# Kernel optimization log

Measured on AMD Instinct MI355X. Metric: run time of the kernel, lower is better.

## Reference

```python
import jax, jax.numpy as jnp
import numpy as np
import math


def _dct2_mat(N):
    # DCT-II matrix, norm=None convention of torch_dct: X[k] = 2*sum_n x[n]*cos(pi*(2n+1)*k/(2N))
    n = np.arange(N)
    k = n[:, None]
    C = 2.0 * np.cos(np.pi * (2 * n[None, :] + 1) * k / (2 * N))
    return jnp.asarray(C, dtype=jnp.float32)


def setup_inputs() -> dict:
    key = jax.random.key(0)
    k1, k2, k3 = jax.random.split(key, 3)
    B, H, W = 128, 256, 256
    thresh = int(H / (2 * math.sqrt(2)))  # 90
    x = jax.random.normal(k1, (B, 3, H, W), dtype=jnp.float32)
    w = jax.random.normal(k2, (1, thresh), dtype=jnp.float32) * 0.05
    b = jax.random.normal(k3, (1,), dtype=jnp.float32) * 0.05
    return {"x": x, "w": w, "b": b}


def reference(x, w, b):
    B, C, H, W = x.shape
    Ch = _dct2_mat(H)
    Cw = _dct2_mat(W)
    # dct_2d: DCT-II along last two dims
    xd = jnp.einsum('bchw,kw->bchk', x, Cw)
    xd = jnp.einsum('bchk,jh->bcjk', xd, Ch)
    xd = jax.lax.stop_gradient(xd)  # original does x.detach() inside get_fft_feature
    gray = 0.2989 * xd[:, 0] + 0.587 * xd[:, 1] + 0.114 * xd[:, 2]  # [B,H,W]
    F = jnp.fft.fft2(gray, axes=(-2, -1))
    re = F.real + 1e-8  # original adds epsilon to both real and imag parts
    im = F.imag + 1e-8
    mag = jnp.log(jnp.sqrt(re * re + im * im + 1e-10) + 1e-10)
    mag = jnp.fft.fftshift(mag, axes=(-2, -1))  # quadrant-swap `shift` == fftshift for even dims
    # radial binning (static integer radii, as in azimuthalAverage)
    yy, xx = np.indices([H, W])
    r = np.sqrt((xx - H / 2) ** 2 + (yy - W / 2) ** 2).astype(np.int32).ravel()
    nbins = int(r.max()) + 1
    nr = jnp.asarray(np.bincount(r, minlength=nbins).astype(np.float32))
    rj = jnp.asarray(r)
    tbin = jax.vmap(lambda m: jax.ops.segment_sum(m, rj, num_segments=nbins))(mag.reshape(B, -1))
    prof = tbin / (nr + 1e-10)  # [B, nbins]
    prof = prof[:, 1:-2]  # azimuthalAverage returns radial_prof[1:-2]
    mn = jnp.min(prof, axis=1, keepdims=True)
    mx = jnp.max(prof, axis=1, keepdims=True)
    out = (prof - mn) / (mx - mn)
    out = jnp.where(jnp.isnan(out), 0.0, out)
    thresh = w.shape[1]
    feat = out[:, -thresh:]  # [B, thresh]
    return feat @ w.T + b  # [B, 1]
```

## Files before the change

### kernel.cpp

```cpp
#include <hip/hip_runtime.h>
#include <math.h>

#define NBINS 182
#define NB 128

typedef unsigned short u16;
typedef __attribute__((ext_vector_type(8))) short short8;
typedef __attribute__((ext_vector_type(4))) float f32x4;

__device__ __forceinline__ u16 f2bf(float f) {
    union { float f; unsigned u; } v; v.f = f;
    unsigned r = v.u + 0x7FFF + ((v.u >> 16) & 1);
    return (u16)(r >> 16);
}
__device__ __forceinline__ float bf2f(u16 u) {
    union { unsigned u; float f; } v; v.u = ((unsigned)u) << 16;
    return v.f;
}
__device__ __forceinline__ short8 negbf(short8 v) {
    short8 r;
#pragma unroll
    for (int i = 0; i < 8; ++i) r[i] = v[i] ^ (short)0x8000;
    return r;
}

__device__ __forceinline__ int radial_bin(int dx, int dy) {
    return (int)sqrtf((float)(dx * dx + dy * dy));
}

__global__ __launch_bounds__(256) void prep(const float* __restrict__ x,
                                            u16* __restrict__ G,
                                            float* __restrict__ M_re,
                                            float* __restrict__ M_im,
                                            u16* __restrict__ A1,
                                            float* __restrict__ nrpart,
                                            float* __restrict__ tbin) {
    __shared__ double ctab[1024];
    __shared__ double stab[1024];
    __shared__ float s[NBINS];
    int blk = blockIdx.x;
    int t = threadIdx.x;

    if (blk < 256) {
        for (int i = t; i < 1024; i += 256) {
            double a = 3.14159265358979323846 * (double)i / 512.0;
            ctab[i] = cos(a);
            stab[i] = sin(a);
        }
        __syncthreads();
        int j = blk;
        int w = t;
        double re = 0.0, im = 0.0;
        int tw = 2 * w + 1;
        for (int k = 0; k < 256; ++k) {
            int e = (4 * j * k) & 1023;
            int m = (tw * k) & 1023;
            double cw = 2.0 * ctab[m];
            re += ctab[e] * cw;
            im -= stab[e] * cw;
        }
        M_re[j * 256 + w] = (float)re;
        M_im[j * 256 + w] = (float)im;
        A1[j * 256 + w] = f2bf((float)re);
        A1[(j + 256) * 256 + w] = f2bf((float)im);
    } else if (blk < 512) {
        int i = blk - 256;
        if (t < NBINS) s[t] = 0.0f;
        __syncthreads();
        int bin = radial_bin(t - 128, i - 128);
        atomicAdd(&s[bin], 1.0f);
        __syncthreads();
        if (t < NBINS) nrpart[t * 256 + i] = s[t];
    } else if (blk < 544) {
        int idx = (blk - 512) * 256 + t;
        for (int i = idx; i < NB * NBINS; i += 32 * 256) tbin[i] = 0.0f;
    } else {
        int tid = (blk - 544) * 256 + t;
        for (int i = tid; i < 2097152; i += 262144) {
            int idx = i * 4;
            int b = idx >> 16;
            int rem = idx & 65535;
            const float* p = x + (size_t)b * 196608 + rem;
            float4 r = *(const float4*)p;
            float4 g = *(const float4*)(p + 65536);
            float4 bl = *(const float4*)(p + 131072);
            float g0 = 0.2989f * r.x + 0.587f * g.x + 0.114f * bl.x;
            float g1 = 0.2989f * r.y + 0.587f * g.y + 0.114f * bl.y;
            float g2 = 0.2989f * r.z + 0.587f * g.z + 0.114f * bl.z;
            float g3 = 0.2989f * r.w + 0.587f * g.w + 0.114f * bl.w;
            uint2 o;
            o.x = (unsigned)f2bf(g0) | ((unsigned)f2bf(g1) << 16);
            o.y = (unsigned)f2bf(g2) | ((unsigned)f2bf(g3) << 16);
            *(uint2*)(G + idx) = o;
        }
    }
}

__global__ __launch_bounds__(256) void s1(const u16* __restrict__ A1,
                                          const u16* __restrict__ G,
                                          u16* __restrict__ Tt_re,
                                          u16* __restrict__ Tt_im) {
    __shared__ u16 As[128 * 40];
    __shared__ u16 Bs[128 * 40];
    __shared__ u16 Cs[64 * 136];
    int b = blockIdx.z;
    int r0 = blockIdx.y * 128;
    int h0 = blockIdx.x * 128;
    int t = threadIdx.x;
    int lane = t & 63, wv = t >> 6;
    int wr = (wv >> 1) * 64;
    int wc = (wv & 1) * 64;
    int fr = lane & 15;
    int fk = (lane >> 4) << 3;

    f32x4 acc[4][4];
#pragma unroll
    for (int i = 0; i < 4; ++i)
#pragma unroll
        for (int j = 0; j < 4; ++j) acc[i][j] = (f32x4){0.f, 0.f, 0.f, 0.f};

    const u16* Ap = A1 + (size_t)r0 * 256;
    const u16* Gp = G + (size_t)b * 65536 + (size_t)h0 * 256;

    for (int kk = 0; kk < 256; kk += 32) {
#pragma unroll
        for (int c = t; c < 512; c += 256) {
            int row = c >> 2, off = (c & 3) << 3;
            *(uint4*)&As[row * 40 + off] =
                *(const uint4*)(Ap + (size_t)row * 256 + kk + off);
            *(uint4*)&Bs[row * 40 + off] =
                *(const uint4*)(Gp + (size_t)row * 256 + kk + off);
        }
        __syncthreads();
        short8 af[4], bfr[4];
#pragma unroll
        for (int i = 0; i < 4; ++i)
            af[i] = *(const short8*)&As[(wr + i * 16 + fr) * 40 + fk];
#pragma unroll
        for (int j = 0; j < 4; ++j)
            bfr[j] = *(const short8*)&Bs[(wc + j * 16 + fr) * 40 + fk];
#pragma unroll
        for (int i = 0; i < 4; ++i)
#pragma unroll
            for (int j = 0; j < 4; ++j)
                acc[i][j] = __builtin_amdgcn_mfma_f32_16x16x32_bf16(
                    af[i], bfr[j], acc[i][j], 0, 0, 0);
        __syncthreads();
    }

    u16* dstp = ((r0 < 256) ? Tt_re : Tt_im) + (size_t)b * 65536
              + (size_t)(r0 & 255) * 256 + h0;
    int rq = (lane >> 4) << 2;
#pragma unroll
    for (int pass = 0; pass < 2; ++pass) {
        if ((wr >> 6) == pass) {
#pragma unroll
            for (int i = 0; i < 4; ++i)
#pragma unroll
                for (int j = 0; j < 4; ++j) {
                    int col = wc + j * 16 + fr;
#pragma unroll
                    for (int reg = 0; reg < 4; ++reg) {
                        int lrow = i * 16 + rq + reg;
                        Cs[lrow * 136 + col] = f2bf(acc[i][j][reg]);
                    }
                }
        }
        __syncthreads();
        for (int idx = t; idx < 1024; idx += 256) {
            int row = idx >> 4, k = idx & 15;
            *(uint4*)(dstp + (size_t)(pass * 64 + row) * 256 + k * 8) =
                *(const uint4*)&Cs[row * 136 + k * 8];
        }
        __syncthreads();
    }
}

__global__ __launch_bounds__(256) void s2f(const u16* __restrict__ A1,
                                           const float* __restrict__ M_re,
                                           const u16* __restrict__ Tt_re,
                                           const u16* __restrict__ Tt_im,
                                           float* __restrict__ tbin) {
    __shared__ u16 Ar[64 * 40], Ai[64 * 40], Br[64 * 40], Bi[64 * 40];
    __shared__ float sbins[NBINS];
    __shared__ float sM[256];
    int blk = blockIdx.x;
    int t = threadIdx.x;

    if (blk >= 1024) {
        int b = blk - 1024;
        sM[t] = M_re[128 * 256 + t];
        __syncthreads();
        if (t > 128) return;
        const u16* pr = Tt_re + (size_t)b * 65536 + (size_t)t * 256;
        const u16* pi = Tt_im + (size_t)b * 65536 + (size_t)t * 256;
        float re = 0.0f, im = 0.0f;
        for (int h = 0; h < 256; h += 8) {
            uint4 vr = *(const uint4*)(pr + h);
            uint4 vi = *(const uint4*)(pi + h);
            unsigned wr[4] = {vr.x, vr.y, vr.z, vr.w};
            unsigned wi[4] = {vi.x, vi.y, vi.z, vi.w};
#pragma unroll
            for (int q = 0; q < 4; ++q) {
                re = fmaf(sM[h + 2 * q], bf2f((u16)(wr[q] & 0xffff)), re);
                re = fmaf(sM[h + 2 * q + 1], bf2f((u16)(wr[q] >> 16)), re);
                im = fmaf(sM[h + 2 * q], bf2f((u16)(wi[q] & 0xffff)), im);
                im = fmaf(sM[h + 2 * q + 1], bf2f((u16)(wi[q] >> 16)), im);
            }
        }
        re += 1e-8f; im += 1e-8f;
        float mag = __logf(sqrtf(re * re + im * im + 1e-10f) + 1e-10f);
        float wj = (t == 0 || t == 128) ? 1.0f : 2.0f;
        int dx = (t < 128) ? t : t - 256;
        int bin = radial_bin(dx, -128);
        atomicAdd(&tbin[b * NBINS + bin], wj * mag);
        return;
    }

    int b = blk >> 3;
    int u0 = ((blk >> 2) & 1) * 64;
    int j0 = (blk & 3) * 64;
    int lane = t & 63, wv = t >> 6;
    int wu = (wv >> 1) * 32;
    int wj = (wv & 1) * 32;
    int fr = lane & 15;
    int fk = (lane >> 4) << 3;

    for (int i = t; i < NBINS; i += 256) sbins[i] = 0.0f;

    f32x4 accr[2][2], acci[2][2];
#pragma unroll
    for (int i = 0; i < 2; ++i)
#pragma unroll
        for (int j = 0; j < 2; ++j) {
            accr[i][j] = (f32x4){0.f, 0.f, 0.f, 0.f};
            acci[i][j] = (f32x4){0.f, 0.f, 0.f, 0.f};
        }

    const u16* Apr = A1 + (size_t)u0 * 256;
    const u16* Api = A1 + (size_t)(256 + u0) * 256;
    const u16* Tr = Tt_re + (size_t)b * 65536 + (size_t)j0 * 256;
    const u16* Ti = Tt_im + (size_t)b * 65536 + (size_t)j0 * 256;

    int lrow = t >> 2, loff = (t & 3) << 3;

    for (int kk = 0; kk < 256; kk += 32) {
        *(uint4*)&Ar[lrow * 40 + loff] =
            *(const uint4*)(Apr + (size_t)lrow * 256 + kk + loff);
        *(uint4*)&Ai[lrow * 40 + loff] =
            *(const uint4*)(Api + (size_t)lrow * 256 + kk + loff);
        *(uint4*)&Br[lrow * 40 + loff] =
            *(const uint4*)(Tr + (size_t)lrow * 256 + kk + loff);
        *(uint4*)&Bi[lrow * 40 + loff] =
            *(const uint4*)(Ti + (size_t)lrow * 256 + kk + loff);
        __syncthreads();
        short8 arf[2], aif[2], naif[2], brf[2], bif[2];
#pragma unroll
        for (int i = 0; i < 2; ++i) {
            arf[i] = *(const short8*)&Ar[(wu + i * 16 + fr) * 40 + fk];
            aif[i] = *(const short8*)&Ai[(wu + i * 16 + fr) * 40 + fk];
            naif[i] = negbf(aif[i]);
        }
#pragma unroll
        for (int j = 0; j < 2; ++j) {
            brf[j] = *(const short8*)&Br[(wj + j * 16 + fr) * 40 + fk];
            bif[j] = *(const short8*)&Bi[(wj + j * 16 + fr) * 40 + fk];
        }
#pragma unroll
        for (int i = 0; i < 2; ++i)
#pragma unroll
            for (int j = 0; j < 2; ++j) {
                accr[i][j] = __builtin_amdgcn_mfma_f32_16x16x32_bf16(
                    arf[i], brf[j], accr[i][j], 0, 0, 0);
                accr[i][j] = __builtin_amdgcn_mfma_f32_16x16x32_bf16(
                    naif[i], bif[j], accr[i][j], 0, 0, 0);
                acci[i][j] = __builtin_amdgcn_mfma_f32_16x16x32_bf16(
                    arf[i], bif[j], acci[i][j], 0, 0, 0);
                acci[i][j] = __builtin_amdgcn_mfma_f32_16x16x32_bf16(
                    aif[i], brf[j], acci[i][j], 0, 0, 0);
            }
        __syncthreads();
    }

    int rq = (lane >> 4) << 2;
#pragma unroll
    for (int i = 0; i < 2; ++i)
#pragma unroll
        for (int j = 0; j < 2; ++j) {
            int v = j0 + wj + j * 16 + fr;
            int dx = (v < 128) ? v : v - 256;
            int dx2 = dx * dx;
#pragma unroll
            for (int reg = 0; reg < 4; ++reg) {
                int u = u0 + wu + i * 16 + rq + reg;
                float wrow = (u == 0) ? 1.0f : 2.0f;
                int bin = (int)sqrtf((float)(dx2 + u * u));
                float re = accr[i][j][reg] + 1e-8f;
                float im = acci[i][j][reg] + 1e-8f;
                float mag = __logf(sqrtf(re * re + im * im + 1e-10f) + 1e-10f);
                atomicAdd(&sbins[bin], wrow * mag);
            }
        }
    __syncthreads();
    for (int i = t; i < NBINS; i += 256)
        atomicAdd(&tbin[b * NBINS + i], sbins[i]);
}

__global__ __launch_bounds__(192) void finalize(const float* __restrict__ tbin,
                                                const float* __restrict__ nrpart,
                                                const float* __restrict__ w,
                                                const float* __restrict__ bias,
                                                float* __restrict__ out) {
    __shared__ float prof[NBINS];
    __shared__ float smn, smx, ssum;
    int b = blockIdx.x;
    int t = threadIdx.x;
    if (t < NBINS) {
        const float4* p = (const float4*)(nrpart + t * 256);
        float4 a = {0.f, 0.f, 0.f, 0.f};
        for (int i = 0; i < 64; ++i) {
            float4 v = p[i];
            a.x += v.x; a.y += v.y; a.z += v.z; a.w += v.w;
        }
        float nr = (a.x + a.y) + (a.z + a.w);
        prof[t] = tbin[b * NBINS + t] / (nr + 1e-10f);
    }
    __syncthreads();
    if (t == 0) {
        float mn = prof[1], mx = prof[1];
        for (int i = 2; i <= 179; ++i) {
            float p = prof[i];
            mn = fminf(mn, p);
            mx = fmaxf(mx, p);
        }
        smn = mn; smx = mx; ssum = 0.0f;
    }
    __syncthreads();
    if (t < 90) {
        float denom = smx - smn;
        float v = (prof[90 + t] - smn) / denom;
        if (v != v) v = 0.0f;
        atomicAdd(&ssum, v * w[t]);
    }
    __syncthreads();
    if (t == 0) out[b] = ssum + bias[0];
}

extern "C" void kernel_launch(void* const* d_in, const int* in_sizes, int n_in,
                              void* d_out, int out_size, void* d_ws, size_t ws_size,
                              hipStream_t stream) {
    const float* x = (const float*)d_in[0];
    const float* w = (const float*)d_in[1];
    const float* bias = (const float*)d_in[2];
    float* out = (float*)d_out;

    float* M_re = (float*)d_ws;
    float* M_im = M_re + 65536;
    u16* A1 = (u16*)(M_im + 65536);
    u16* G = A1 + 131072;
    u16* Tt_re = G + (size_t)NB * 65536;
    u16* Tt_im = Tt_re + (size_t)NB * 65536;
    float* tbin = (float*)(Tt_im + (size_t)NB * 65536);
    float* nrpart = tbin + NB * NBINS;

    prep<<<1568, 256, 0, stream>>>(x, G, M_re, M_im, A1, nrpart, tbin);
    s1<<<dim3(2, 4, NB), 256, 0, stream>>>(A1, G, Tt_re, Tt_im);
    s2f<<<1152, 256, 0, stream>>>(A1, M_re, Tt_re, Tt_im, tbin);
    finalize<<<NB, 192, 0, stream>>>(tbin, nrpart, w, bias, out);
}
```

Baseline: 233.4 us.

## Fuse grayscale into first DCT GEMM and finalize into second stage

The grayscale bf16 conversion moves out of the prep kernel and into the s1 GEMM's B-tile load, so the intermediate G buffer is no longer written and re-read. s1 now stores its results straight from the accumulators to global memory instead of staging them through LDS. The finalize kernel is merged into s2f: each block bumps a per-batch counter and the last one computes the profile and output. The trade-offs are that x is re-read by each row-tile block, the stores become narrow and scattered, and the completion counter adds atomics and fences.

Measured after the change: 317.9 us. 36.2% more time.

```diff
diff --git a/kernel.cpp b/kernel.cpp
--- a/kernel.cpp
+++ b/kernel.cpp
@@ -28,13 +28,12 @@
     return (int)sqrtf((float)(dx * dx + dy * dy));
 }
 
-__global__ __launch_bounds__(256) void prep(const float* __restrict__ x,
-                                            u16* __restrict__ G,
-                                            float* __restrict__ M_re,
+__global__ __launch_bounds__(256) void prep(float* __restrict__ M_re,
                                             float* __restrict__ M_im,
                                             u16* __restrict__ A1,
                                             float* __restrict__ nrpart,
-                                            float* __restrict__ tbin) {
+                                            float* __restrict__ tbin,
+                                            int* __restrict__ cnt) {
     __shared__ double ctab[1024];
     __shared__ double stab[1024];
     __shared__ float s[NBINS];
@@ -71,16 +70,51 @@
         atomicAdd(&s[bin], 1.0f);
         __syncthreads();
         if (t < NBINS) nrpart[t * 256 + i] = s[t];
-    } else if (blk < 544) {
+    } else {
         int idx = (blk - 512) * 256 + t;
         for (int i = idx; i < NB * NBINS; i += 32 * 256) tbin[i] = 0.0f;
-    } else {
-        int tid = (blk - 544) * 256 + t;
-        for (int i = tid; i < 2097152; i += 262144) {
-            int idx = i * 4;
-            int b = idx >> 16;
-            int rem = idx & 65535;
-            const float* p = x + (size_t)b * 196608 + rem;
+        if (blk == 512 && t < NB) cnt[t] = 0;
+    }
+}
+
+__global__ __launch_bounds__(256) void s1(const float* __restrict__ x,
+                                          const u16* __restrict__ A1,
+                                          u16* __restrict__ Tt_re,
+                                          u16* __restrict__ Tt_im) {
+    __shared__ u16 As[128 * 40];
+    __shared__ u16 Bs[128 * 40];
+    int b = blockIdx.z;
+    int r0 = blockIdx.y * 128;
+    int h0 = blockIdx.x * 128;
+    int t = threadIdx.x;
+    int lane = t & 63, wv = t >> 6;
+    int wr = (wv >> 1) * 64;
+    int wc = (wv & 1) * 64;
+    int fr = lane & 15;
+    int fk = (lane >> 4) << 3;
+
+    f32x4 acc[4][4];
+#pragma unroll
+    for (int i = 0; i < 4; ++i)
+#pragma unroll
+        for (int j = 0; j < 4; ++j) acc[i][j] = (f32x4){0.f, 0.f, 0.f, 0.f};
+
+    const u16* Ap = A1 + (size_t)r0 * 256;
+    const float* xb = x + (size_t)b * 196608 + (size_t)h0 * 256;
+
+    for (int kk = 0; kk < 256; kk += 32) {
+#pragma unroll
+        for (int c = t; c < 512; c += 256) {
+            int row = c >> 2, off = (c & 3) << 3;
+            *(uint4*)&As[row * 40 + off] =
+                *(const uint4*)(Ap + (size_t)row * 256 + kk + off);
+        }
+#pragma unroll
+        for (int it = 0; it < 4; ++it) {
+            int id = t + it * 256;
+            int row = id >> 3;
+            int cg = (id & 7) * 4;
+            const float* p = xb + (size_t)row * 256 + kk + cg;
             float4 r = *(const float4*)p;
             float4 g = *(const float4*)(p + 65536);
             float4 bl = *(const float4*)(p + 131072);
@@ -91,45 +125,7 @@
             uint2 o;
             o.x = (unsigned)f2bf(g0) | ((unsigned)f2bf(g1) << 16);
             o.y = (unsigned)f2bf(g2) | ((unsigned)f2bf(g3) << 16);
-            *(uint2*)(G + idx) = o;
-        }
-    }
-}
-
-__global__ __launch_bounds__(256) void s1(const u16* __restrict__ A1,
-                                          const u16* __restrict__ G,
-                                          u16* __restrict__ Tt_re,
-                                          u16* __restrict__ Tt_im) {
-    __shared__ u16 As[128 * 40];
-    __shared__ u16 Bs[128 * 40];
-    __shared__ u16 Cs[64 * 136];
-    int b = blockIdx.z;
-    int r0 = blockIdx.y * 128;
-    int h0 = blockIdx.x * 128;
-    int t = threadIdx.x;
-    int lane = t & 63, wv = t >> 6;
-    int wr = (wv >> 1) * 64;
-    int wc = (wv & 1) * 64;
-    int fr = lane & 15;
-    int fk = (lane >> 4) << 3;
-
-    f32x4 acc[4][4];
-#pragma unroll
-    for (int i = 0; i < 4; ++i)
-#pragma unroll
-        for (int j = 0; j < 4; ++j) acc[i][j] = (f32x4){0.f, 0.f, 0.f, 0.f};
-
-    const u16* Ap = A1 + (size_t)r0 * 256;
-    const u16* Gp = G + (size_t)b * 65536 + (size_t)h0 * 256;
-
-    for (int kk = 0; kk < 256; kk += 32) {
-#pragma unroll
-        for (int c = t; c < 512; c += 256) {
-            int row = c >> 2, off = (c & 3) << 3;
-            *(uint4*)&As[row * 40 + off] =
-                *(const uint4*)(Ap + (size_t)row * 256 + kk + off);
-            *(uint4*)&Bs[row * 40 + off] =
-                *(const uint4*)(Gp + (size_t)row * 256 + kk + off);
+            *(uint2*)&Bs[row * 40 + cg] = o;
         }
         __syncthreads();
         short8 af[4], bfr[4];
@@ -148,173 +144,166 @@
         __syncthreads();
     }
 
-    u16* dstp = ((r0 < 256) ? Tt_re : Tt_im) + (size_t)b * 65536
-              + (size_t)(r0 & 255) * 256 + h0;
+    u16* dst = ((r0 < 256) ? Tt_re : Tt_im) + (size_t)b * 65536
+             + (size_t)(r0 & 255) * 256;
     int rq = (lane >> 4) << 2;
 #pragma unroll
-    for (int pass = 0; pass < 2; ++pass) {
-        if ((wr >> 6) == pass) {
-#pragma unroll
-            for (int i = 0; i < 4; ++i)
-#pragma unroll
-                for (int j = 0; j < 4; ++j) {
-                    int col = wc + j * 16 + fr;
-#pragma unroll
-                    for (int reg = 0; reg < 4; ++reg) {
-                        int lrow = i * 16 + rq + reg;
-                        Cs[lrow * 136 + col] = f2bf(acc[i][j][reg]);
-                    }
-                }
-        }
-        __syncthreads();
-        for (int idx = t; idx < 1024; idx += 256) {
-            int row = idx >> 4, k = idx & 15;
-            *(uint4*)(dstp + (size_t)(pass * 64 + row) * 256 + k * 8) =
-                *(const uint4*)&Cs[row * 136 + k * 8];
-        }
-        __syncthreads();
-    }
+    for (int i = 0; i < 4; ++i)
+#pragma unroll
+        for (int j = 0; j < 4; ++j) {
+            int col = h0 + wc + j * 16 + fr;
+#pragma unroll
+            for (int reg = 0; reg < 4; ++reg) {
+                int row = wr + i * 16 + rq + reg;
+                dst[(size_t)row * 256 + col] = f2bf(acc[i][j][reg]);
+            }
+        }
 }
 
 __global__ __launch_bounds__(256) void s2f(const u16* __restrict__ A1,
                                            const float* __restrict__ M_re,
                                            const u16* __restrict__ Tt_re,
                                            const u16* __restrict__ Tt_im,
-                                           float* __restrict__ tbin) {
+                                           float* __restrict__ tbin,
+                                           const float* __restrict__ nrpart,
+                                           const float* __restrict__ w,
+                                           const float* __restrict__ bias,
+                                           float* __restrict__ out,
+                                           int* __restrict__ cnt) {
     __shared__ u16 Ar[64 * 40], Ai[64 * 40], Br[64 * 40], Bi[64 * 40];
     __shared__ float sbins[NBINS];
     __shared__ float sM[256];
+    __shared__ float prof[NBINS];
+    __shared__ float smn, smx, ssum;
+    __shared__ int sdone;
     int blk = blockIdx.x;
     int t = threadIdx.x;
+    int b;
 
     if (blk >= 1024) {
-        int b = blk - 1024;
+        b = blk - 1024;
         sM[t] = M_re[128 * 256 + t];
         __syncthreads();
-        if (t > 128) return;
-        const u16* pr = Tt_re + (size_t)b * 65536 + (size_t)t * 256;
-        const u16* pi = Tt_im + (size_t)b * 65536 + (size_t)t * 256;
-        float re = 0.0f, im = 0.0f;
-        for (int h = 0; h < 256; h += 8) {
-            uint4 vr = *(const uint4*)(pr + h);
-            uint4 vi = *(const uint4*)(pi + h);
-            unsigned wr[4] = {vr.x, vr.y, vr.z, vr.w};
-            unsigned wi[4] = {vi.x, vi.y, vi.z, vi.w};
-#pragma unroll
-            for (int q = 0; q < 4; ++q) {
-                re = fmaf(sM[h + 2 * q], bf2f((u16)(wr[q] & 0xffff)), re);
-                re = fmaf(sM[h + 2 * q + 1], bf2f((u16)(wr[q] >> 16)), re);
-                im = fmaf(sM[h + 2 * q], bf2f((u16)(wi[q] & 0xffff)), im);
-                im = fmaf(sM[h + 2 * q + 1], bf2f((u16)(wi[q] >> 16)), im);
-            }
-        }
-        re += 1e-8f; im += 1e-8f;
-        float mag = __logf(sqrtf(re * re + im * im + 1e-10f) + 1e-10f);
-        float wj = (t == 0 || t == 128) ? 1.0f : 2.0f;
-        int dx = (t < 128) ? t : t - 256;
-        int bin = radial_bin(dx, -128);
-        atomicAdd(&tbin[b * NBINS + bin], wj * mag);
-        return;
-    }
-
-    int b = blk >> 3;
-    int u0 = ((blk >> 2) & 1) * 64;
-    int j0 = (blk & 3) * 64;
-    int lane = t & 63, wv = t >> 6;
-    int wu = (wv >> 1) * 32;
-    int wj = (wv & 1) * 32;
-    int fr = lane & 15;
-    int fk = (lane >> 4) << 3;
-
-    for (int i = t; i < NBINS; i += 256) sbins[i] = 0.0f;
-
-    f32x4 accr[2][2], acci[2][2];
-#pragma unroll
-    for (int i = 0; i < 2; ++i)
-#pragma unroll
-        for (int j = 0; j < 2; ++j) {
-            accr[i][j] = (f32x4){0.f, 0.f, 0.f, 0.f};
-            acci[i][j] = (f32x4){0.f, 0.f, 0.f, 0.f};
-        }
-
-    const u16* Apr = A1 + (size_t)u0 * 256;
-    const u16* Api = A1 + (size_t)(256 + u0) * 256;
-    const u16* Tr = Tt_re + (size_t)b * 65536 + (size_t)j0 * 256;
-    const u16* Ti = Tt_im + (size_t)b * 65536 + (size_t)j0 * 256;
-
-    int lrow = t >> 2, loff = (t & 3) << 3;
-
-    for (int kk = 0; kk < 256; kk += 32) {
-        *(uint4*)&Ar[lrow * 40 + loff] =
-            *(const uint4*)(Apr + (size_t)lrow * 256 + kk + loff);
-        *(uint4*)&Ai[lrow * 40 + loff] =
-            *(const uint4*)(Api + (size_t)lrow * 256 + kk + loff);
-        *(uint4*)&Br[lrow * 40 + loff] =
-            *(const uint4*)(Tr + (size_t)lrow * 256 + kk + loff);
-        *(uint4*)&Bi[lrow * 40 + loff] =
-            *(const uint4*)(Ti + (size_t)lrow * 256 + kk + loff);
-        __syncthreads();
-        short8 arf[2], aif[2], naif[2], brf[2], bif[2];
-#pragma unroll
-        for (int i = 0; i < 2; ++i) {
-            arf[i] = *(const short8*)&Ar[(wu + i * 16 + fr) * 40 + fk];
-            aif[i] = *(const short8*)&Ai[(wu + i * 16 + fr) * 40 + fk];
-            naif[i] = negbf(aif[i]);
-        }
-#pragma unroll
-        for (int j = 0; j < 2; ++j) {
-            brf[j] = *(const short8*)&Br[(wj + j * 16 + fr) * 40 + fk];
-            bif[j] = *(const short8*)&Bi[(wj + j * 16 + fr) * 40 + fk];
-        }
+        if (t <= 128) {
+            const u16* pr = Tt_re + (size_t)b * 65536 + (size_t)t * 256;
+            const u16* pi = Tt_im + (size_t)b * 65536 + (size_t)t * 256;
+            float re = 0.0f, im = 0.0f;
+            for (int h = 0; h < 256; h += 8) {
+                uint4 vr = *(const uint4*)(pr + h);
+                uint4 vi = *(const uint4*)(pi + h);
+                unsigned wr[4] = {vr.x, vr.y, vr.z, vr.w};
+                unsigned wi[4] = {vi.x, vi.y, vi.z, vi.w};
+#pragma unroll
+                for (int q = 0; q < 4; ++q) {
+                    re = fmaf(sM[h + 2 * q], bf2f((u16)(wr[q] & 0xffff)), re);
+                    re = fmaf(sM[h + 2 * q + 1], bf2f((u16)(wr[q] >> 16)), re);
+                    im = fmaf(sM[h + 2 * q], bf2f((u16)(wi[q] & 0xffff)), im);
+                    im = fmaf(sM[h + 2 * q + 1], bf2f((u16)(wi[q] >> 16)), im);
+                }
+            }
+            re += 1e-8f; im += 1e-8f;
+            float mag = __logf(sqrtf(re * re + im * im + 1e-10f) + 1e-10f);
+            float wj = (t == 0 || t == 128) ? 1.0f : 2.0f;
+            int dx = (t < 128) ? t : t - 256;
+            int bin = radial_bin(dx, -128);
+            atomicAdd(&tbin[b * NBINS + bin], wj * mag);
+        }
+    } else {
+        b = blk >> 3;
+        int u0 = ((blk >> 2) & 1) * 64;
+        int j0 = (blk & 3) * 64;
+        int lane = t & 63, wv = t >> 6;
+        int wu = (wv >> 1) * 32;
+        int wj = (wv & 1) * 32;
+        int fr = lane & 15;
+        int fk = (lane >> 4) << 3;
+
+        for (int i = t; i < NBINS; i += 256) sbins[i] = 0.0f;
+
+        f32x4 accr[2][2], acci[2][2];
 #pragma unroll
         for (int i = 0; i < 2; ++i)
 #pragma unroll
             for (int j = 0; j < 2; ++j) {
-                accr[i][j] = __builtin_amdgcn_mfma_f32_16x16x32_bf16(
-                    arf[i], brf[j], accr[i][j], 0, 0, 0);
-                accr[i][j] = __builtin_amdgcn_mfma_f32_16x16x32_bf16(
-                    naif[i], bif[j], accr[i][j], 0, 0, 0);
-                acci[i][j] = __builtin_amdgcn_mfma_f32_16x16x32_bf16(
-                    arf[i], bif[j], acci[i][j], 0, 0, 0);
-                acci[i][j] = __builtin_amdgcn_mfma_f32_16x16x32_bf16(
-                    aif[i], brf[j], acci[i][j], 0, 0, 0);
-            }
-        __syncthreads();
-    }
-
-    int rq = (lane >> 4) << 2;
-#pragma unroll
-    for (int i = 0; i < 2; ++i)
-#pragma unroll
-        for (int j = 0; j < 2; ++j) {
-            int v = j0 + wj + j * 16 + fr;
-            int dx = (v < 128) ? v : v - 256;
-            int dx2 = dx * dx;
-#pragma unroll
-            for (int reg = 0; reg < 4; ++reg) {
-                int u = u0 + wu + i * 16 + rq + reg;
-                float wrow = (u == 0) ? 1.0f : 2.0f;
-                int bin = (int)sqrtf((float)(dx2 + u * u));
-                float re = accr[i][j][reg] + 1e-8f;
-                float im = acci[i][j][reg] + 1e-8f;
-                float mag = __logf(sqrtf(re * re + im * im + 1e-10f) + 1e-10f);
-                atomicAdd(&sbins[bin], wrow * mag);
-            }
-        }
-    __syncthreads();
-    for (int i = t; i < NBINS; i += 256)
-        atomicAdd(&tbin[b * NBINS + i], sbins[i]);
-}
-
-__global__ __launch_bounds__(192) void finalize(const float* __restrict__ tbin,
-                                                const float* __restrict__ nrpart,
-                                                const float* __restrict__ w,
-                                                const float* __restrict__ bias,
-                                                float* __restrict__ out) {
-    __shared__ float prof[NBINS];
-    __shared__ float smn, smx, ssum;
-    int b = blockIdx.x;
-    int t = threadIdx.x;
+                accr[i][j] = (f32x4){0.f, 0.f, 0.f, 0.f};
+                acci[i][j] = (f32x4){0.f, 0.f, 0.f, 0.f};
+            }
+
+        const u16* Apr = A1 + (size_t)u0 * 256;
+        const u16* Api = A1 + (size_t)(256 + u0) * 256;
+        const u16* Tr = Tt_re + (size_t)b * 65536 + (size_t)j0 * 256;
+        const u16* Ti = Tt_im + (size_t)b * 65536 + (size_t)j0 * 256;
+
+        int lrow = t >> 2, loff = (t & 3) << 3;
+
+        for (int kk = 0; kk < 256; kk += 32) {
+            *(uint4*)&Ar[lrow * 40 + loff] =
+                *(const uint4*)(Apr + (size_t)lrow * 256 + kk + loff);
+            *(uint4*)&Ai[lrow * 40 + loff] =
+                *(const uint4*)(Api + (size_t)lrow * 256 + kk + loff);
+            *(uint4*)&Br[lrow * 40 + loff] =
+                *(const uint4*)(Tr + (size_t)lrow * 256 + kk + loff);
+            *(uint4*)&Bi[lrow * 40 + loff] =
+                *(const uint4*)(Ti + (size_t)lrow * 256 + kk + loff);
+            __syncthreads();
+            short8 arf[2], aif[2], naif[2], brf[2], bif[2];
+#pragma unroll
+            for (int i = 0; i < 2; ++i) {
+                arf[i] = *(const short8*)&Ar[(wu + i * 16 + fr) * 40 + fk];
+                aif[i] = *(const short8*)&Ai[(wu + i * 16 + fr) * 40 + fk];
+                naif[i] = negbf(aif[i]);
+            }
+#pragma unroll
+            for (int j = 0; j < 2; ++j) {
+                brf[j] = *(const short8*)&Br[(wj + j * 16 + fr) * 40 + fk];
+                bif[j] = *(const short8*)&Bi[(wj + j * 16 + fr) * 40 + fk];
+            }
+#pragma unroll
+            for (int i = 0; i < 2; ++i)
+#pragma unroll
+                for (int j = 0; j < 2; ++j) {
+                    accr[i][j] = __builtin_amdgcn_mfma_f32_16x16x32_bf16(
+                        arf[i], brf[j], accr[i][j], 0, 0, 0);
+                    accr[i][j] = __builtin_amdgcn_mfma_f32_16x16x32_bf16(
+                        naif[i], bif[j], accr[i][j], 0, 0, 0);
+                    acci[i][j] = __builtin_amdgcn_mfma_f32_16x16x32_bf16(
+                        arf[i], bif[j], acci[i][j], 0, 0, 0);
+                    acci[i][j] = __builtin_amdgcn_mfma_f32_16x16x32_bf16(
+                        aif[i], brf[j], acci[i][j], 0, 0, 0);
+                }
+            __syncthreads();
+        }
+
+        int rq = (lane >> 4) << 2;
+#pragma unroll
+        for (int i = 0; i < 2; ++i)
+#pragma unroll
+            for (int j = 0; j < 2; ++j) {
+                int v = j0 + wj + j * 16 + fr;
+                int dx = (v < 128) ? v : v - 256;
+                int dx2 = dx * dx;
+#pragma unroll
+                for (int reg = 0; reg < 4; ++reg) {
+                    int u = u0 + wu + i * 16 + rq + reg;
+                    float wrow = (u == 0) ? 1.0f : 2.0f;
+                    int bin = (int)sqrtf((float)(dx2 + u * u));
+                    float re = accr[i][j][reg] + 1e-8f;
+                    float im = acci[i][j][reg] + 1e-8f;
+                    float mag = __logf(sqrtf(re * re + im * im + 1e-10f) + 1e-10f);
+                    atomicAdd(&sbins[bin], wrow * mag);
+                }
+            }
+        __syncthreads();
+        for (int i = t; i < NBINS; i += 256)
+            atomicAdd(&tbin[b * NBINS + i], sbins[i]);
+    }
+
+    __threadfence();
+    __syncthreads();
+    if (t == 0) sdone = atomicAdd(&cnt[b], 1);
+    __syncthreads();
+    if (sdone != 8) return;
+
     if (t < NBINS) {
         const float4* p = (const float4*)(nrpart + t * 256);
         float4 a = {0.f, 0.f, 0.f, 0.f};
@@ -323,7 +312,9 @@
             a.x += v.x; a.y += v.y; a.z += v.z; a.w += v.w;
         }
         float nr = (a.x + a.y) + (a.z + a.w);
-        prof[t] = tbin[b * NBINS + t] / (nr + 1e-10f);
+        float tb = __hip_atomic_load(&tbin[b * NBINS + t], __ATOMIC_RELAXED,
+                                     __HIP_MEMORY_SCOPE_AGENT);
+        prof[t] = tb / (nr + 1e-10f);
     }
     __syncthreads();
     if (t == 0) {
@@ -357,14 +348,14 @@
     float* M_re = (float*)d_ws;
     float* M_im = M_re + 65536;
     u16* A1 = (u16*)(M_im + 65536);
-    u16* G = A1 + 131072;
-    u16* Tt_re = G + (size_t)NB * 65536;
+    u16* Tt_re = A1 + 131072;
     u16* Tt_im = Tt_re + (size_t)NB * 65536;
     float* tbin = (float*)(Tt_im + (size_t)NB * 65536);
     float* nrpart = tbin + NB * NBINS;
-
-    prep<<<1568, 256, 0, stream>>>(x, G, M_re, M_im, A1, nrpart, tbin);
-    s1<<<dim3(2, 4, NB), 256, 0, stream>>>(A1, G, Tt_re, Tt_im);
-    s2f<<<1152, 256, 0, stream>>>(A1, M_re, Tt_re, Tt_im, tbin);
-    finalize<<<NB, 192, 0, stream>>>(tbin, nrpart, w, bias, out);
-}
+    int* cnt = (int*)(nrpart + NBINS * 256);
+
+    prep<<<544, 256, 0, stream>>>(M_re, M_im, A1, nrpart, tbin, cnt);
+    s1<<<dim3(2, 4, NB), 256, 0, stream>>>(x, A1, Tt_re, Tt_im);
+    s2f<<<1152, 256, 0, stream>>>(A1, M_re, Tt_re, Tt_im, tbin, nrpart,
+                                  w, bias, out, cnt);
+}
```
